# Optimization experiments

Measured on AMD Instinct MI355X. Metric: run time of the kernel, lower is better.

The kernel has to match this reference:

```python
import jax, jax.numpy as jnp
from jax import lax
import numpy as np

B, T, A = 128, 2048, 3
H = 100  # LSTM units
F = 64   # conv filters


def setup_inputs() -> dict:
    key = jax.random.key(0)
    ks = jax.random.split(key, 8)
    s = lambda k, shape, scale: (jax.random.normal(k, shape, dtype=jnp.float32) * scale)
    return {
        "state_input": s(ks[0], (B, T, 1), 1.0),
        "conv_w": s(ks[1], (2, 1, F), 0.5),
        "conv_b": jnp.zeros((F,), jnp.float32),
        "lstm1_w": s(ks[2], (F, 4 * H), 0.08),
        "lstm1_u": s(ks[3], (H, 4 * H), 0.08),
        "lstm1_b": jnp.zeros((4 * H,), jnp.float32),
        "lstm2_w": s(ks[4], (H, 4 * H), 0.08),
        "lstm2_u": s(ks[5], (H, 4 * H), 0.08),
        "lstm2_b": jnp.zeros((4 * H,), jnp.float32),
        "dense_w": s(ks[6], (H, A), 0.1),
        "dense_b": jnp.zeros((A,), jnp.float32),
    }


def _lstm_relu(x, W, U, b, return_sequences):
    # Keras LSTM with activation='relu', recurrent_activation='sigmoid'.
    # Gate order: i, f, g(candidate), o. h = o * relu(c).
    Bz = x.shape[0]
    xz = jnp.einsum("btf,fg->btg", x, W) + b  # precompute input projections [B,T,4H]
    h0 = jnp.zeros((Bz, U.shape[0]), x.dtype)
    c0 = jnp.zeros_like(h0)

    def step(carry, xz_t):
        h, c = carry
        z = xz_t + h @ U
        i, f, g, o = jnp.split(z, 4, axis=-1)
        i = jax.nn.sigmoid(i)
        f = jax.nn.sigmoid(f)
        g = jax.nn.relu(g)
        o = jax.nn.sigmoid(o)
        c = f * c + i * g
        h = o * jax.nn.relu(c)
        return (h, c), (h if return_sequences else 0.0)

    (h_last, _), hs = lax.scan(step, (h0, c0), jnp.swapaxes(xz, 0, 1))
    if return_sequences:
        return jnp.swapaxes(hs, 0, 1)  # [B,T,H]
    return h_last


def reference(state_input, conv_w, conv_b, lstm1_w, lstm1_u, lstm1_b,
              lstm2_w, lstm2_u, lstm2_b, dense_w, dense_b):
    # Conv1D(filters=64, kernel_size=2, padding='valid', relu): [B,T,1]->[B,T-1,64]
    x = lax.conv_general_dilated(
        state_input, conv_w, window_strides=(1,), padding="VALID",
        dimension_numbers=("NWC", "WIO", "NWC"))
    x = jax.nn.relu(x + conv_b)
    # MaxPool1D(pool_size=1) is the identity.
    x = _lstm_relu(x, lstm1_w, lstm1_u, lstm1_b, return_sequences=True)
    # Dropout at inference is identity.
    x = _lstm_relu(x, lstm2_w, lstm2_u, lstm2_b, return_sequences=False)  # [B,H]
    logits = x @ dense_w + dense_b
    return jax.nn.softmax(logits, axis=-1)
```

## Files before the change

kernel.cpp:

```cpp
#include <hip/hip_runtime.h>
#include <math.h>


typedef _Float16 h2 __attribute__((ext_vector_type(2)));

#define TT 2048
#define TP 2047
#define HH 100
#define G4 400
#define FF 64
#define NB 128

#define X1R 176
#define CBQ 104
#define NPW (400 * 88)
#define NCW (400 * 100)
#define CHK 64
#define NCHUNK 32
#define RINGC 4
#define CHUNK_DW (CHK * 50)

#define WS_FLAGS (NPW + NCW)
#define WS_RING  (WS_FLAGS + 256)

#define FD2(w, xs, acc) acc = __builtin_amdgcn_fdot2(w, xs, acc, false)
#define B2(f) __builtin_bit_cast(h2, f)

static __device__ __forceinline__ float psum2(float z) {
    int p = __builtin_amdgcn_update_dpp(0, __builtin_bit_cast(int, z),
                                        0xB1, 0xF, 0xF, true);
    return z + __builtin_bit_cast(float, p);
}
static __device__ __forceinline__ float xswap2(float z) {
    int p = __builtin_amdgcn_update_dpp(0, __builtin_bit_cast(int, z),
                                        0x4E, 0xF, 0xF, true);
    return __builtin_bit_cast(float, p);
}
static __device__ __forceinline__ float sig(float z) {
    return 1.0f / (1.0f + __expf(-z));
}
static __device__ __forceinline__ void step_barrier() {
    __builtin_amdgcn_sched_barrier(0);
    asm volatile("s_waitcnt lgkmcnt(0)" ::: "memory");
    __builtin_amdgcn_sched_barrier(0);
    __builtin_amdgcn_s_barrier();
    __builtin_amdgcn_sched_barrier(0);
}

__global__ void prep_weights(const float* __restrict__ w1, const float* __restrict__ u1,
                             const float* __restrict__ w2, const float* __restrict__ u2,
                             h2* __restrict__ ws)
{
    const int idx = blockIdx.x * 256 + threadIdx.x;
    if (idx >= NPW + NCW) return;
    float lo = 0.f, hi = 0.f;
    if (idx < NPW) {
        const int rt = idx / 88, r = idx % 88;
        const int qq = (r >> 2) * 2 + ((r & 3) >> 1);
        const int gs = r & 1;
        const int p = rt >> 2, g2 = (rt >> 1) & 1, kh = rt & 1;
        const int col = (2 * g2 + gs) * HH + p;
        const int E0 = 2 * qq;
#pragma unroll
        for (int e = 0; e < 2; ++e) {
            const int E = E0 + e;
            float v = 0.f;
            if (E < 82) {
                const int k = kh * 82 + E;
                v = (k < FF) ? w1[k * G4 + col] : u1[(k - FF) * G4 + col];
            }
            if (e == 0) lo = v; else hi = v;
        }
    } else {
        const int i2 = idx - NPW;
        const int rt = i2 / 100, r = i2 % 100;
        const int qq = (r >> 2) * 2 + ((r & 3) >> 1);
        const int gs = r & 1;
        const int p = rt >> 2, g2 = (rt >> 1) & 1, kh = rt & 1;
        const int col = (2 * g2 + gs) * HH + p;
        const int k0 = 2 * qq;
        const float* M = kh ? u2 : w2;
        lo = M[k0 * G4 + col];
        hi = M[(k0 + 1) * G4 + col];
    }
    ws[idx] = h2{(_Float16)lo, (_Float16)hi};
}

__global__ __launch_bounds__(512, 2)
void fused_lstm_kernel(const float* __restrict__ s,
                       const float* __restrict__ conv_w,
                       const float* __restrict__ conv_b,
                       const float* __restrict__ b1,
                       const float* __restrict__ b2,
                       const float* __restrict__ dw, const float* __restrict__ db,
                       h2* __restrict__ wpk,
                       float* __restrict__ out)
{
    const int tid  = threadIdx.x;
    const int bb   = blockIdx.x;
    const int b    = bb & (NB - 1);
    const bool prod = bb < NB;

    int* pflag = (int*)(wpk + WS_FLAGS) + b;
    int* aflag = (int*)(wpk + WS_FLAGS) + 128 + b;
    unsigned* ring = (unsigned*)(wpk + WS_RING) + (size_t)b * (RINGC * CHUNK_DW);

    __shared__ float s_buf[TT];
    __shared__ __align__(16) _Float16 X1[2 * X1R];
    __shared__ __align__(16) _Float16 CB[CHK * CBQ];
    __shared__ __align__(16) _Float16 HR[2 * CBQ];

    if (prod) {
        for (int i = tid; i < TT; i += 512) s_buf[i] = s[(size_t)b * TT + i];
        if (tid < X1R) ((unsigned*)X1)[tid] = 0u;
    } else {
        if (tid < CBQ) ((unsigned*)HR)[tid] = 0u;
        if (tid < CHK * 2)
            ((unsigned*)CB)[(tid >> 1) * 52 + 50 + (tid & 1)] = 0u;
    }
    __syncthreads();

    if (prod) {
        if (tid < 448) {
            const int rt = tid;
            const int active = rt < 400;
            const int lrt = active ? rt : 0;
            const int p  = lrt >> 2;
            const int g2 = (lrt >> 1) & 1;
            const int kh = lrt & 1;
            const int cL = (2 * g2) * HH + p;

            h2 wa[44], wb[44];
            {
                const float4* w4 = (const float4*)(wpk + (size_t)lrt * 88);
#pragma unroll
                for (int j = 0; j < 22; ++j) {
                    const float4 v = w4[j];
                    wa[2*j]   = B2(v.x); wb[2*j]   = B2(v.y);
                    wa[2*j+1] = B2(v.z); wb[2*j+1] = B2(v.w);
                }
            }
            const float bL = b1[cL], bH = b1[cL + HH];
            const int hoff = (p < 18) ? (64 + p) : (p + 70);
            __syncthreads();

            float c = 0.0f;
            for (int t = 0; t < TP; ++t) {
                if ((t & 63) == 0) {
                    const int k = t >> 6;
                    if (tid == 0 && k >= RINGC) {
                        int g = 0;
                        while (__hip_atomic_load(aflag, __ATOMIC_ACQUIRE,
                                                 __HIP_MEMORY_SCOPE_AGENT) < k - (RINGC - 1)
                               && g < 50000000) { ++g; __builtin_amdgcn_s_sleep(8); }
                    }
                    __syncthreads();
                }
                if (active) {
                    _Float16* cur = X1 + (t & 1) * X1R;
                    _Float16* nx1 = X1 + ((t & 1) ^ 1) * X1R;
                    float za0 = 0.f, za1 = 0.f, zb0 = 0.f, zb1 = 0.f;
                    const float4* vb = (const float4*)(cur + kh * 88);
#pragma unroll
                    for (int r2 = 0; r2 < 11; ++r2) {
                        const float4 v = vb[r2];
                        FD2(wa[4*r2+0], B2(v.x), za0); FD2(wb[4*r2+0], B2(v.x), zb0);
                        FD2(wa[4*r2+1], B2(v.y), za1); FD2(wb[4*r2+1], B2(v.y), zb1);
                        FD2(wa[4*r2+2], B2(v.z), za0); FD2(wb[4*r2+2], B2(v.z), zb0);
                        FD2(wa[4*r2+3], B2(v.w), za1); FD2(wb[4*r2+3], B2(v.w), zb1);
                    }
                    const float zaS = psum2(za0 + za1) + bL;
                    const float zbS = psum2(zb0 + zb1) + bH;
                    const float oa = xswap2(zaS), ob = xswap2(zbS);
                    const float zi = g2 ? oa  : zaS;
                    const float zf = g2 ? ob  : zbS;
                    const float zg = g2 ? zaS : oa;
                    const float zo = g2 ? zbS : ob;
                    c = fmaf(sig(zf), c, sig(zi) * fmaxf(zg, 0.f));
                    const float h = sig(zo) * fmaxf(c, 0.f);
                    if ((rt & 3) == 0) {
                        const _Float16 hq = (_Float16)h;
                        nx1[hoff] = hq;
                        const unsigned hb = (unsigned)__builtin_bit_cast(unsigned short, hq);
                        const unsigned prt =
                            (unsigned)__builtin_amdgcn_ds_swizzle((int)hb, 0x101F) & 0xFFFFu;
                        if (!(p & 1))
                            __hip_atomic_store(ring + ((t >> 6) & 3) * CHUNK_DW
                                                    + (t & 63) * 50 + (p >> 1),
                                               hb | (prt << 16), __ATOMIC_RELAXED,
                                               __HIP_MEMORY_SCOPE_AGENT);
                    }
                    if (((t & 63) == 63) || (t == TP - 1))
                        asm volatile("s_waitcnt vmcnt(0)" ::: "memory");
                }
                step_barrier();
                if (tid == 0 && (((t & 63) == 63) || (t == TP - 1)))
                    __hip_atomic_fetch_add(pflag, 1, __ATOMIC_RELEASE,
                                           __HIP_MEMORY_SCOPE_AGENT);
            }
        } else {
            const int f = tid - 448;
            const float cv0 = conv_w[f], cv1 = conv_w[FF + f], cb0 = conv_b[f];
            X1[f] = (_Float16)fmaxf(fmaf(s_buf[0], cv0, fmaf(s_buf[1], cv1, cb0)), 0.f);
            __syncthreads();
            for (int t = 0; t < TP; ++t) {
                if ((t & 63) == 0) __syncthreads();
                if (t + 1 < TP) {
                    _Float16* nx1 = X1 + ((t & 1) ^ 1) * X1R;
                    nx1[f] = (_Float16)fmaxf(
                        fmaf(s_buf[t + 1], cv0, fmaf(s_buf[t + 2], cv1, cb0)), 0.f);
                }
                step_barrier();
            }
        }
    } else {
        if (tid < 448) {
            const int rt = tid;
            const int active = rt < 400;
            const int lrt = active ? rt : 0;
            const int p  = lrt >> 2;
            const int g2 = (lrt >> 1) & 1;
            const int kh = lrt & 1;
            const int cL = (2 * g2) * HH + p;

            h2 wa[50], wb[50];
            {
                const float4* w4 = (const float4*)(wpk + NPW + (size_t)lrt * 100);
#pragma unroll
                for (int j = 0; j < 25; ++j) {
                    const float4 v = w4[j];
                    wa[2*j]   = B2(v.x); wb[2*j]   = B2(v.y);
                    wa[2*j+1] = B2(v.z); wb[2*j+1] = B2(v.w);
                }
            }
            const float bL = b2[cL], bH = b2[cL + HH];
            __syncthreads();

            float c = 0.0f;
            for (int k = 0; k < NCHUNK; ++k) {
                if (tid == 0) {
                    int g = 0;
                    while (__hip_atomic_load(pflag, __ATOMIC_ACQUIRE,
                                             __HIP_MEMORY_SCOPE_AGENT) < k + 1
                           && g < 50000000) { ++g; __builtin_amdgcn_s_sleep(8); }
                }
                __syncthreads();
                const int csz = (TP - (k << 6) < CHK) ? (TP - (k << 6)) : CHK;
                unsigned* gsrc = ring + (k & 3) * CHUNK_DW;
                for (int d = tid; d < csz * 50; d += 448)
                    ((unsigned*)CB)[(d / 50) * 52 + (d % 50)] =
                        __hip_atomic_load(gsrc + d, __ATOMIC_RELAXED,
                                          __HIP_MEMORY_SCOPE_AGENT);
                __syncthreads();
                if (tid == 0)
                    __hip_atomic_fetch_add(aflag, 1, __ATOMIC_RELAXED,
                                           __HIP_MEMORY_SCOPE_AGENT);
                for (int lt = 0; lt < csz; ++lt) {
                    const int t = (k << 6) + lt;
                    if (active) {
                        const _Float16* base = kh ? (HR + (t & 1) * CBQ)
                                                  : (CB + lt * CBQ);
                        float za0 = 0.f, za1 = 0.f, zb0 = 0.f, zb1 = 0.f;
                        const float4* vb = (const float4*)base;
#pragma unroll
                        for (int r2 = 0; r2 < 12; ++r2) {
                            const float4 v = vb[r2];
                            FD2(wa[4*r2+0], B2(v.x), za0); FD2(wb[4*r2+0], B2(v.x), zb0);
                            FD2(wa[4*r2+1], B2(v.y), za1); FD2(wb[4*r2+1], B2(v.y), zb1);
                            FD2(wa[4*r2+2], B2(v.z), za0); FD2(wb[4*r2+2], B2(v.z), zb0);
                            FD2(wa[4*r2+3], B2(v.w), za1); FD2(wb[4*r2+3], B2(v.w), zb1);
                        }
                        {
                            const float2 tv = *(const float2*)(base + 96);
                            FD2(wa[48], B2(tv.x), za0); FD2(wb[48], B2(tv.x), zb0);
                            FD2(wa[49], B2(tv.y), za1); FD2(wb[49], B2(tv.y), zb1);
                        }
                        const float zaS = psum2(za0 + za1) + bL;
                        const float zbS = psum2(zb0 + zb1) + bH;
                        const float oa = xswap2(zaS), ob = xswap2(zbS);
                        const float zi = g2 ? oa  : zaS;
                        const float zf = g2 ? ob  : zbS;
                        const float zg = g2 ? zaS : oa;
                        const float zo = g2 ? zbS : ob;
                        c = fmaf(sig(zf), c, sig(zi) * fmaxf(zg, 0.f));
                        const float h = sig(zo) * fmaxf(c, 0.f);
                        if ((rt & 3) == 0)
                            HR[((t & 1) ^ 1) * CBQ + p] = (_Float16)h;
                    }
                    step_barrier();
                }
            }

            if (rt == 0) {
                float l[3];
#pragma unroll
                for (int a = 0; a < 3; ++a) {
                    float acc = db[a];
                    for (int j = 0; j < HH; ++j)
                        acc = fmaf((float)HR[CBQ + j], dw[j * 3 + a], acc);
                    l[a] = acc;
                }
                const float m = fmaxf(l[0], fmaxf(l[1], l[2]));
                const float e0 = __expf(l[0] - m), e1 = __expf(l[1] - m), e2 = __expf(l[2] - m);
                const float inv = 1.0f / (e0 + e1 + e2);
                out[b * 3 + 0] = e0 * inv;
                out[b * 3 + 1] = e1 * inv;
                out[b * 3 + 2] = e2 * inv;
            }
        } else {
            __syncthreads();
            for (int k = 0; k < NCHUNK; ++k) {
                __syncthreads();
                const int csz = (TP - (k << 6) < CHK) ? (TP - (k << 6)) : CHK;
                __syncthreads();
                for (int lt = 0; lt < csz; ++lt)
                    step_barrier();
            }
        }
    }
}

extern "C" void kernel_launch(void* const* d_in, const int* in_sizes, int n_in,
                              void* d_out, int out_size, void* d_ws, size_t ws_size,
                              hipStream_t stream) {
    const float* s      = (const float*)d_in[0];
    const float* conv_w = (const float*)d_in[1];
    const float* conv_b = (const float*)d_in[2];
    const float* w1     = (const float*)d_in[3];
    const float* u1     = (const float*)d_in[4];
    const float* b1     = (const float*)d_in[5];
    const float* w2     = (const float*)d_in[6];
    const float* u2     = (const float*)d_in[7];
    const float* b2     = (const float*)d_in[8];
    const float* dw     = (const float*)d_in[9];
    const float* db     = (const float*)d_in[10];

    h2* ws = (h2*)d_ws;
    hipMemsetAsync((void*)((int*)(ws + WS_FLAGS)), 0, 256 * sizeof(int), stream);
    const int nh2 = NPW + NCW;
    prep_weights<<<(nh2 + 255) / 256, 256, 0, stream>>>(w1, u1, w2, u2, ws);
    fused_lstm_kernel<<<256, 512, 0, stream>>>(
        s, conv_w, conv_b, b1, b2, dw, db, ws, (float*)d_out);
}
```

Before: 1.845 ms.

## Process two batch rows per block to amortize register-held weights and barriers

Each producer and consumer block now handles two batch elements instead of one, so the grid shrinks from 256 to 128 blocks. Every thread reuses its register-resident fp16 weights for two dot products per step, and the per-step barrier count and fixed step latency are shared across both sequences. Shared buffers and ring traffic are doubled per block. The cost is more work on each block's serial critical path per timestep and occupancy of only one block per CU, with launch bounds relaxed to allow more registers.

```diff
diff --git a/kernel.cpp b/kernel.cpp
--- a/kernel.cpp
+++ b/kernel.cpp
@@ -9,7 +9,7 @@
 #define HH 100
 #define G4 400
 #define FF 64
-#define NB 128
+#define PB 64
 
 #define X1R 176
 #define CBQ 104
@@ -86,7 +86,41 @@
     ws[idx] = h2{(_Float16)lo, (_Float16)hi};
 }
 
-__global__ __launch_bounds__(512, 2)
+#define CDOT(base, za0, za1, zb0, zb1) { \
+    const float4* vb = (const float4*)(base); \
+_Pragma("unroll") \
+    for (int r2 = 0; r2 < 12; ++r2) { \
+        const float4 v = vb[r2]; \
+        FD2(wa[4*r2+0], B2(v.x), za0); FD2(wb[4*r2+0], B2(v.x), zb0); \
+        FD2(wa[4*r2+1], B2(v.y), za1); FD2(wb[4*r2+1], B2(v.y), zb1); \
+        FD2(wa[4*r2+2], B2(v.z), za0); FD2(wb[4*r2+2], B2(v.z), zb0); \
+        FD2(wa[4*r2+3], B2(v.w), za1); FD2(wb[4*r2+3], B2(v.w), zb1); \
+    } \
+    { const float2 tv = *(const float2*)((base) + 96); \
+      FD2(wa[48], B2(tv.x), za0); FD2(wb[48], B2(tv.x), zb0); \
+      FD2(wa[49], B2(tv.y), za1); FD2(wb[49], B2(tv.y), zb1); } }
+
+#define PDOT(base, za0, za1, zb0, zb1) { \
+    const float4* vb = (const float4*)(base); \
+_Pragma("unroll") \
+    for (int r2 = 0; r2 < 11; ++r2) { \
+        const float4 v = vb[r2]; \
+        FD2(wa[4*r2+0], B2(v.x), za0); FD2(wb[4*r2+0], B2(v.x), zb0); \
+        FD2(wa[4*r2+1], B2(v.y), za1); FD2(wb[4*r2+1], B2(v.y), zb1); \
+        FD2(wa[4*r2+2], B2(v.z), za0); FD2(wb[4*r2+2], B2(v.z), zb0); \
+        FD2(wa[4*r2+3], B2(v.w), za1); FD2(wb[4*r2+3], B2(v.w), zb1); \
+    } }
+
+#define GCELL(zaS, zbS, bLv, bHv, cc, hh_) { \
+    const float oa = xswap2(zaS), ob = xswap2(zbS); \
+    const float zi = g2 ? oa  : zaS; \
+    const float zf = g2 ? ob  : zbS; \
+    const float zg = g2 ? zaS : oa; \
+    const float zo = g2 ? zbS : ob; \
+    cc = fmaf(sig(zf), cc, sig(zi) * fmaxf(zg, 0.f)); \
+    hh_ = sig(zo) * fmaxf(cc, 0.f); }
+
+__global__ __launch_bounds__(512, 1)
 void fused_lstm_kernel(const float* __restrict__ s,
                        const float* __restrict__ conv_w,
                        const float* __restrict__ conv_b,
@@ -98,25 +132,32 @@
 {
     const int tid  = threadIdx.x;
     const int bb   = blockIdx.x;
-    const int b    = bb & (NB - 1);
-    const bool prod = bb < NB;
-
-    int* pflag = (int*)(wpk + WS_FLAGS) + b;
-    int* aflag = (int*)(wpk + WS_FLAGS) + 128 + b;
-    unsigned* ring = (unsigned*)(wpk + WS_RING) + (size_t)b * (RINGC * CHUNK_DW);
-
-    __shared__ float s_buf[TT];
-    __shared__ __align__(16) _Float16 X1[2 * X1R];
-    __shared__ __align__(16) _Float16 CB[CHK * CBQ];
-    __shared__ __align__(16) _Float16 HR[2 * CBQ];
+    const bool prod = bb < PB;
+    const int pr   = prod ? bb : bb - PB;
+    const int b0   = 2 * pr, b1i = 2 * pr + 1;
+
+    int* pflag = (int*)(wpk + WS_FLAGS) + pr;
+    int* aflag = (int*)(wpk + WS_FLAGS) + 128 + pr;
+    unsigned* ring0 = (unsigned*)(wpk + WS_RING) + (size_t)b0  * (RINGC * CHUNK_DW);
+    unsigned* ring1 = (unsigned*)(wpk + WS_RING) + (size_t)b1i * (RINGC * CHUNK_DW);
+
+    __shared__ float s_buf[2 * TT];
+    __shared__ __align__(16) _Float16 X1[4 * X1R];
+    __shared__ __align__(16) _Float16 CB[2 * CHK * CBQ];
+    __shared__ __align__(16) _Float16 HR[4 * CBQ];
 
     if (prod) {
-        for (int i = tid; i < TT; i += 512) s_buf[i] = s[(size_t)b * TT + i];
-        if (tid < X1R) ((unsigned*)X1)[tid] = 0u;
+        for (int i = tid; i < 2 * TT; i += 512) {
+            const int bat = i >> 11, off = i & (TT - 1);
+            s_buf[i] = s[(size_t)(2 * pr + bat) * TT + off];
+        }
+        if (tid < 2 * X1R) ((unsigned*)X1)[tid] = 0u;
     } else {
-        if (tid < CBQ) ((unsigned*)HR)[tid] = 0u;
-        if (tid < CHK * 2)
-            ((unsigned*)CB)[(tid >> 1) * 52 + 50 + (tid & 1)] = 0u;
+        if (tid < 2 * CBQ) ((unsigned*)HR)[tid] = 0u;
+        if (tid < CHK * 4) {
+            const int bat = tid & 1, r = tid >> 2, e = (tid >> 1) & 1;
+            ((unsigned*)(CB + bat * CHK * CBQ))[r * 52 + 50 + e] = 0u;
+        }
     }
     __syncthreads();
 
@@ -144,7 +185,7 @@
             const int hoff = (p < 18) ? (64 + p) : (p + 70);
             __syncthreads();
 
-            float c = 0.0f;
+            float cA = 0.0f, cB2 = 0.0f;
             for (int t = 0; t < TP; ++t) {
                 if ((t & 63) == 0) {
                     const int k = t >> 6;
@@ -157,38 +198,37 @@
                     __syncthreads();
                 }
                 if (active) {
-                    _Float16* cur = X1 + (t & 1) * X1R;
-                    _Float16* nx1 = X1 + ((t & 1) ^ 1) * X1R;
-                    float za0 = 0.f, za1 = 0.f, zb0 = 0.f, zb1 = 0.f;
-                    const float4* vb = (const float4*)(cur + kh * 88);
-#pragma unroll
-                    for (int r2 = 0; r2 < 11; ++r2) {
-                        const float4 v = vb[r2];
-                        FD2(wa[4*r2+0], B2(v.x), za0); FD2(wb[4*r2+0], B2(v.x), zb0);
-                        FD2(wa[4*r2+1], B2(v.y), za1); FD2(wb[4*r2+1], B2(v.y), zb1);
-                        FD2(wa[4*r2+2], B2(v.z), za0); FD2(wb[4*r2+2], B2(v.z), zb0);
-                        FD2(wa[4*r2+3], B2(v.w), za1); FD2(wb[4*r2+3], B2(v.w), zb1);
-                    }
-                    const float zaS = psum2(za0 + za1) + bL;
-                    const float zbS = psum2(zb0 + zb1) + bH;
-                    const float oa = xswap2(zaS), ob = xswap2(zbS);
-                    const float zi = g2 ? oa  : zaS;
-                    const float zf = g2 ? ob  : zbS;
-                    const float zg = g2 ? zaS : oa;
-                    const float zo = g2 ? zbS : ob;
-                    c = fmaf(sig(zf), c, sig(zi) * fmaxf(zg, 0.f));
-                    const float h = sig(zo) * fmaxf(c, 0.f);
+                    const int cs = (t & 1) * X1R, ns = ((t & 1) ^ 1) * X1R;
+                    float zaA0 = 0.f, zaA1 = 0.f, zbA0 = 0.f, zbA1 = 0.f;
+                    float zaB0 = 0.f, zaB1 = 0.f, zbB0 = 0.f, zbB1 = 0.f;
+                    PDOT(X1 + cs + kh * 88, zaA0, zaA1, zbA0, zbA1)
+                    PDOT(X1 + 2 * X1R + cs + kh * 88, zaB0, zaB1, zbB0, zbB1)
+                    const float zaSA = psum2(zaA0 + zaA1) + bL;
+                    const float zbSA = psum2(zbA0 + zbA1) + bH;
+                    const float zaSB = psum2(zaB0 + zaB1) + bL;
+                    const float zbSB = psum2(zbB0 + zbB1) + bH;
+                    float hA, hB;
+                    GCELL(zaSA, zbSA, bL, bH, cA, hA)
+                    GCELL(zaSB, zbSB, bL, bH, cB2, hB)
                     if ((rt & 3) == 0) {
-                        const _Float16 hq = (_Float16)h;
-                        nx1[hoff] = hq;
-                        const unsigned hb = (unsigned)__builtin_bit_cast(unsigned short, hq);
-                        const unsigned prt =
-                            (unsigned)__builtin_amdgcn_ds_swizzle((int)hb, 0x101F) & 0xFFFFu;
-                        if (!(p & 1))
-                            __hip_atomic_store(ring + ((t >> 6) & 3) * CHUNK_DW
-                                                    + (t & 63) * 50 + (p >> 1),
-                                               hb | (prt << 16), __ATOMIC_RELAXED,
-                                               __HIP_MEMORY_SCOPE_AGENT);
+                        const _Float16 hqA = (_Float16)hA;
+                        const _Float16 hqB = (_Float16)hB;
+                        X1[ns + hoff] = hqA;
+                        X1[2 * X1R + ns + hoff] = hqB;
+                        const unsigned hbA = (unsigned)__builtin_bit_cast(unsigned short, hqA);
+                        const unsigned hbB = (unsigned)__builtin_bit_cast(unsigned short, hqB);
+                        const unsigned prtA =
+                            (unsigned)__builtin_amdgcn_ds_swizzle((int)hbA, 0x101F) & 0xFFFFu;
+                        const unsigned prtB =
+                            (unsigned)__builtin_amdgcn_ds_swizzle((int)hbB, 0x101F) & 0xFFFFu;
+                        if (!(p & 1)) {
+                            const size_t roff = (size_t)((t >> 6) & 3) * CHUNK_DW
+                                              + (t & 63) * 50 + (p >> 1);
+                            __hip_atomic_store(ring0 + roff, hbA | (prtA << 16),
+                                               __ATOMIC_RELAXED, __HIP_MEMORY_SCOPE_AGENT);
+                            __hip_atomic_store(ring1 + roff, hbB | (prtB << 16),
+                                               __ATOMIC_RELAXED, __HIP_MEMORY_SCOPE_AGENT);
+                        }
                     }
                     if (((t & 63) == 63) || (t == TP - 1))
                         asm volatile("s_waitcnt vmcnt(0)" ::: "memory");
@@ -202,13 +242,17 @@
             const int f = tid - 448;
             const float cv0 = conv_w[f], cv1 = conv_w[FF + f], cb0 = conv_b[f];
             X1[f] = (_Float16)fmaxf(fmaf(s_buf[0], cv0, fmaf(s_buf[1], cv1, cb0)), 0.f);
+            X1[2 * X1R + f] = (_Float16)fmaxf(
+                fmaf(s_buf[TT], cv0, fmaf(s_buf[TT + 1], cv1, cb0)), 0.f);
             __syncthreads();
             for (int t = 0; t < TP; ++t) {
                 if ((t & 63) == 0) __syncthreads();
                 if (t + 1 < TP) {
-                    _Float16* nx1 = X1 + ((t & 1) ^ 1) * X1R;
-                    nx1[f] = (_Float16)fmaxf(
+                    const int ns = ((t & 1) ^ 1) * X1R;
+                    X1[ns + f] = (_Float16)fmaxf(
                         fmaf(s_buf[t + 1], cv0, fmaf(s_buf[t + 2], cv1, cb0)), 0.f);
+                    X1[2 * X1R + ns + f] = (_Float16)fmaxf(
+                        fmaf(s_buf[TT + t + 1], cv0, fmaf(s_buf[TT + t + 2], cv1, cb0)), 0.f);
                 }
                 step_barrier();
             }
@@ -236,7 +280,7 @@
             const float bL = b2[cL], bH = b2[cL + HH];
             __syncthreads();
 
-            float c = 0.0f;
+            float cA = 0.0f, cB2 = 0.0f;
             for (int k = 0; k < NCHUNK; ++k) {
                 if (tid == 0) {
                     int g = 0;
@@ -246,11 +290,17 @@
                 }
                 __syncthreads();
                 const int csz = (TP - (k << 6) < CHK) ? (TP - (k << 6)) : CHK;
-                unsigned* gsrc = ring + (k & 3) * CHUNK_DW;
-                for (int d = tid; d < csz * 50; d += 448)
-                    ((unsigned*)CB)[(d / 50) * 52 + (d % 50)] =
-                        __hip_atomic_load(gsrc + d, __ATOMIC_RELAXED,
-                                          __HIP_MEMORY_SCOPE_AGENT);
+                unsigned* gsA = ring0 + (k & 3) * CHUNK_DW;
+                unsigned* gsB = ring1 + (k & 3) * CHUNK_DW;
+                unsigned* cbA = (unsigned*)CB;
+                unsigned* cbB = (unsigned*)(CB + CHK * CBQ);
+                for (int d = tid; d < csz * 50; d += 448) {
+                    const int dst = (d / 50) * 52 + (d % 50);
+                    cbA[dst] = __hip_atomic_load(gsA + d, __ATOMIC_RELAXED,
+                                                 __HIP_MEMORY_SCOPE_AGENT);
+                    cbB[dst] = __hip_atomic_load(gsB + d, __ATOMIC_RELAXED,
+                                                 __HIP_MEMORY_SCOPE_AGENT);
+                }
                 __syncthreads();
                 if (tid == 0)
                     __hip_atomic_fetch_add(aflag, 1, __ATOMIC_RELAXED,
@@ -258,54 +308,47 @@
                 for (int lt = 0; lt < csz; ++lt) {
                     const int t = (k << 6) + lt;
                     if (active) {
-                        const _Float16* base = kh ? (HR + (t & 1) * CBQ)
-                                                  : (CB + lt * CBQ);
-                        float za0 = 0.f, za1 = 0.f, zb0 = 0.f, zb1 = 0.f;
-                        const float4* vb = (const float4*)base;
-#pragma unroll
-                        for (int r2 = 0; r2 < 12; ++r2) {
-                            const float4 v = vb[r2];
-                            FD2(wa[4*r2+0], B2(v.x), za0); FD2(wb[4*r2+0], B2(v.x), zb0);
-                            FD2(wa[4*r2+1], B2(v.y), za1); FD2(wb[4*r2+1], B2(v.y), zb1);
-                            FD2(wa[4*r2+2], B2(v.z), za0); FD2(wb[4*r2+2], B2(v.z), zb0);
-                            FD2(wa[4*r2+3], B2(v.w), za1); FD2(wb[4*r2+3], B2(v.w), zb1);
+                        const _Float16* baseA = kh ? (HR + (t & 1) * CBQ)
+                                                   : (CB + lt * CBQ);
+                        const _Float16* baseB = kh ? (HR + 2 * CBQ + (t & 1) * CBQ)
+                                                   : (CB + CHK * CBQ + lt * CBQ);
+                        float zaA0 = 0.f, zaA1 = 0.f, zbA0 = 0.f, zbA1 = 0.f;
+                        float zaB0 = 0.f, zaB1 = 0.f, zbB0 = 0.f, zbB1 = 0.f;
+                        CDOT(baseA, zaA0, zaA1, zbA0, zbA1)
+                        CDOT(baseB, zaB0, zaB1, zbB0, zbB1)
+                        const float zaSA = psum2(zaA0 + zaA1) + bL;
+                        const float zbSA = psum2(zbA0 + zbA1) + bH;
+                        const float zaSB = psum2(zaB0 + zaB1) + bL;
+                        const float zbSB = psum2(zbB0 + zbB1) + bH;
+                        float hA, hB;
+                        GCELL(zaSA, zbSA, bL, bH, cA, hA)
+                        GCELL(zaSB, zbSB, bL, bH, cB2, hB)
+                        if ((rt & 3) == 0) {
+                            HR[((t & 1) ^ 1) * CBQ + p] = (_Float16)hA;
+                            HR[2 * CBQ + ((t & 1) ^ 1) * CBQ + p] = (_Float16)hB;
                         }
-                        {
-                            const float2 tv = *(const float2*)(base + 96);
-                            FD2(wa[48], B2(tv.x), za0); FD2(wb[48], B2(tv.x), zb0);
-                            FD2(wa[49], B2(tv.y), za1); FD2(wb[49], B2(tv.y), zb1);
-                        }
-                        const float zaS = psum2(za0 + za1) + bL;
-                        const float zbS = psum2(zb0 + zb1) + bH;
-                        const float oa = xswap2(zaS), ob = xswap2(zbS);
-                        const float zi = g2 ? oa  : zaS;
-                        const float zf = g2 ? ob  : zbS;
-                        const float zg = g2 ? zaS : oa;
-                        const float zo = g2 ? zbS : ob;
-                        c = fmaf(sig(zf), c, sig(zi) * fmaxf(zg, 0.f));
-                        const float h = sig(zo) * fmaxf(c, 0.f);
-                        if ((rt & 3) == 0)
-                            HR[((t & 1) ^ 1) * CBQ + p] = (_Float16)h;
                     }
                     step_barrier();
                 }
             }
 
-            if (rt == 0) {
+            if (rt < 2) {
+                const _Float16* hf = HR + rt * 2 * CBQ + CBQ;
                 float l[3];
 #pragma unroll
                 for (int a = 0; a < 3; ++a) {
                     float acc = db[a];
                     for (int j = 0; j < HH; ++j)
-                        acc = fmaf((float)HR[CBQ + j], dw[j * 3 + a], acc);
+                        acc = fmaf((float)hf[j], dw[j * 3 + a], acc);
                     l[a] = acc;
                 }
                 const float m = fmaxf(l[0], fmaxf(l[1], l[2]));
                 const float e0 = __expf(l[0] - m), e1 = __expf(l[1] - m), e2 = __expf(l[2] - m);
                 const float inv = 1.0f / (e0 + e1 + e2);
-                out[b * 3 + 0] = e0 * inv;
-                out[b * 3 + 1] = e1 * inv;
-                out[b * 3 + 2] = e2 * inv;
+                const int bo = 2 * pr + rt;
+                out[bo * 3 + 0] = e0 * inv;
+                out[bo * 3 + 1] = e1 * inv;
+                out[bo * 3 + 2] = e2 * inv;
             }
         } else {
             __syncthreads();
@@ -339,6 +382,6 @@
     hipMemsetAsync((void*)((int*)(ws + WS_FLAGS)), 0, 256 * sizeof(int), stream);
     const int nh2 = NPW + NCW;
     prep_weights<<<(nh2 + 255) / 256, 256, 0, stream>>>(w1, u1, w2, u2, ws);
-    fused_lstm_kernel<<<256, 512, 0, stream>>>(
+    fused_lstm_kernel<<<2 * PB, 512, 0, stream>>>(
         s, conv_w, conv_b, b1, b2, dw, db, ws, (float*)d_out);
 }
```

After: 3.156 ms. 1.71x slower.
